# Kernel optimization log

Measured on AMD Instinct MI355X. Metric: run time of the kernel, lower is better.

## Reference

```python
import jax, jax.numpy as jnp
import numpy as np

N, E, D, C = 40000, 640000, 128, 64


def setup_inputs() -> dict:
    key = jax.random.key(0)
    ks = jax.random.split(key, 12)
    x = jax.random.normal(ks[0], (N, D), dtype=jnp.float32)
    edge_row = jax.random.randint(ks[1], (E,), 0, N, dtype=jnp.int32)
    edge_col = jax.random.randint(ks[2], (E,), 0, N, dtype=jnp.int32)
    edge_val = jax.random.uniform(ks[3], (E,), dtype=jnp.float32)
    s1 = 1.0 / np.sqrt(D)
    W1 = jax.random.uniform(ks[4], (D, D), minval=-s1, maxval=s1, dtype=jnp.float32)
    b1 = jax.random.uniform(ks[5], (D,), minval=-s1, maxval=s1, dtype=jnp.float32)
    W2 = jax.random.uniform(ks[6], (D, D), minval=-s1, maxval=s1, dtype=jnp.float32)
    b2 = jax.random.uniform(ks[7], (D,), minval=-s1, maxval=s1, dtype=jnp.float32)
    Wf = jax.random.uniform(ks[8], (D, C), minval=-s1, maxval=s1, dtype=jnp.float32)
    bf = jax.random.uniform(ks[9], (C,), minval=-s1, maxval=s1, dtype=jnp.float32)
    return {"x": x, "edge_row": edge_row, "edge_col": edge_col, "edge_val": edge_val,
            "W1": W1, "b1": b1, "W2": W2, "b2": b2, "Wf": Wf, "bf": bf}


def _spmm(row, col, val, dense):
    # out[row] += val * dense[col]  == adj @ dense with adj in COO form
    msgs = dense[col] * val[:, None]  # [E, D]
    return jax.ops.segment_sum(msgs, row, num_segments=N)


def reference(x, edge_row, edge_col, edge_val, W1, b1, W2, b2, Wf, bf):
    # gc1: relu(adj @ (x @ W1) + b1)
    h = jax.nn.relu(_spmm(edge_row, edge_col, edge_val, x @ W1) + b1)
    # dropout(p=0.2, training=False) -> identity in eval mode
    # gc2 + residual: relu(adj @ (h @ W2) + b2) + h
    h2 = jax.nn.relu(_spmm(edge_row, edge_col, edge_val, h @ W2) + b2) + h
    # final linear classifier
    return h2 @ Wf + bf
```

## Files before the change

### kernel.cpp

```cpp
#include <hip/hip_runtime.h>

#define N_NODES 40000
#define N_EDGES 640000
#define DIM     128
#define NCLS    64
#define CAP     64
#define CSTRIDE 16

typedef __attribute__((ext_vector_type(8))) short short8v;
typedef __attribute__((ext_vector_type(4))) float f32x4;

__device__ __forceinline__ unsigned short f2bf(float f) {
    unsigned int u = __float_as_uint(f);
    unsigned int r = u + 0x7fffu + ((u >> 16) & 1u);
    return (unsigned short)(r >> 16);
}
__device__ __forceinline__ float bf2f(unsigned int s) {
    return __uint_as_float(s << 16);
}

__launch_bounds__(256)
__global__ void prep(const float4* __restrict__ x4, uint2* __restrict__ xb,
                     const float* __restrict__ W1, const float* __restrict__ W2,
                     const float* __restrict__ Wf,
                     unsigned short* __restrict__ wt1, unsigned short* __restrict__ wt2,
                     unsigned short* __restrict__ wtf, int* __restrict__ counts) {
    const int b = blockIdx.x, tid = threadIdx.x;
    if (b < 5000) {
        int i = b * 256 + tid;
        float4 v = x4[i];
        uint2 o;
        o.x = (unsigned)f2bf(v.x) | ((unsigned)f2bf(v.y) << 16);
        o.y = (unsigned)f2bf(v.z) | ((unsigned)f2bf(v.w) << 16);
        xb[i] = o;
    } else if (b < 7500) {
        counts[(b - 5000) * 256 + tid] = 0;
    } else if (b < 7564) {
        int e = (b - 7500) * 256 + tid;
        int k = e >> 7, n = e & 127;
        wt1[n * 128 + k] = f2bf(W1[e]);
    } else if (b < 7628) {
        int e = (b - 7564) * 256 + tid;
        int k = e >> 7, n = e & 127;
        wt2[n * 128 + k] = f2bf(W2[e]);
    } else {
        int e = (b - 7628) * 256 + tid;
        int k = e >> 6, n = e & 63;
        wtf[n * 128 + k] = f2bf(Wf[e]);
    }
}

__launch_bounds__(256)
__global__ void build_bucket(const int* __restrict__ erow, const int* __restrict__ ecol,
                             const float* __restrict__ evalv, int* __restrict__ counts,
                             uint2* __restrict__ bslot) {
    int e = blockIdx.x * blockDim.x + threadIdx.x;
    if (e >= N_EDGES) return;
    int r = erow[e];
    int p = atomicAdd(&counts[r * CSTRIDE], 1);
    if (p < CAP)
        bslot[(size_t)r * CAP + p] = make_uint2((unsigned)ecol[e], __float_as_uint(evalv[e]));
}

__launch_bounds__(256)
__global__ void gemm_bf16_128(const unsigned short* __restrict__ A,
                              const unsigned short* __restrict__ WT,
                              unsigned short* __restrict__ C) {
    __shared__ unsigned short sB[128 * 128];
    const int tid = threadIdx.x;
    for (int c = tid; c < 2048; c += 256) {
        int n = c >> 4, j = c & 15;
        short8v v = *reinterpret_cast<const short8v*>(WT + n * 128 + 8 * j);
        *reinterpret_cast<short8v*>(&sB[n * 128 + 8 * (j ^ (n & 7))]) = v;
    }
    __syncthreads();

    const int lane = tid & 63;
    const int wv   = tid >> 6;
    const int m0   = blockIdx.x * 64 + wv * 16;
    const int r    = lane & 15;
    const int g    = lane >> 4;

    short8v af[4];
    const unsigned short* arow = A + (size_t)(m0 + r) * 128 + 8 * g;
#pragma unroll
    for (int f = 0; f < 4; ++f)
        af[f] = *reinterpret_cast<const short8v*>(arow + 32 * f);

    f32x4 acc[8];
#pragma unroll
    for (int nt = 0; nt < 8; ++nt) acc[nt] = (f32x4){0.f, 0.f, 0.f, 0.f};

#pragma unroll
    for (int nt = 0; nt < 8; ++nt) {
        const int rw = nt * 16 + r;
        const unsigned short* bbase = &sB[rw * 128];
#pragma unroll
        for (int f = 0; f < 4; ++f) {
            short8v bfr = *reinterpret_cast<const short8v*>(bbase + 8 * ((4 * f + g) ^ (rw & 7)));
            acc[nt] = __builtin_amdgcn_mfma_f32_16x16x32_bf16(af[f], bfr, acc[nt], 0, 0, 0);
        }
    }
#pragma unroll
    for (int nt = 0; nt < 8; ++nt)
#pragma unroll
        for (int rr = 0; rr < 4; ++rr)
            C[(size_t)(m0 + g * 4 + rr) * 128 + nt * 16 + r] = f2bf(acc[nt][rr]);
}

__launch_bounds__(256)
__global__ void gemm_bf16_final(const unsigned short* __restrict__ A,
                                const unsigned short* __restrict__ WT,
                                const float* __restrict__ bias,
                                float* __restrict__ C) {
    __shared__ unsigned short sB[64 * 128];
    const int tid = threadIdx.x;
    for (int c = tid; c < 1024; c += 256) {
        int n = c >> 4, j = c & 15;
        short8v v = *reinterpret_cast<const short8v*>(WT + n * 128 + 8 * j);
        *reinterpret_cast<short8v*>(&sB[n * 128 + 8 * (j ^ (n & 7))]) = v;
    }
    __syncthreads();

    const int lane = tid & 63;
    const int wv   = tid >> 6;
    const int m0   = blockIdx.x * 64 + wv * 16;
    const int r    = lane & 15;
    const int g    = lane >> 4;

    short8v af[4];
    const unsigned short* arow = A + (size_t)(m0 + r) * 128 + 8 * g;
#pragma unroll
    for (int f = 0; f < 4; ++f)
        af[f] = *reinterpret_cast<const short8v*>(arow + 32 * f);

    f32x4 acc[4];
#pragma unroll
    for (int nt = 0; nt < 4; ++nt) acc[nt] = (f32x4){0.f, 0.f, 0.f, 0.f};

#pragma unroll
    for (int nt = 0; nt < 4; ++nt) {
        const int rw = nt * 16 + r;
        const unsigned short* bbase = &sB[rw * 128];
#pragma unroll
        for (int f = 0; f < 4; ++f) {
            short8v bfr = *reinterpret_cast<const short8v*>(bbase + 8 * ((4 * f + g) ^ (rw & 7)));
            acc[nt] = __builtin_amdgcn_mfma_f32_16x16x32_bf16(af[f], bfr, acc[nt], 0, 0, 0);
        }
    }
#pragma unroll
    for (int nt = 0; nt < 4; ++nt)
#pragma unroll
        for (int rr = 0; rr < 4; ++rr)
            C[(size_t)(m0 + g * 4 + rr) * 64 + nt * 16 + r] = acc[nt][rr] + bias[nt * 16 + r];
}

__launch_bounds__(256)
__global__ void spmm_fused_bf16(const unsigned int* __restrict__ dense,
                                const uint2* __restrict__ bslot,
                                const int* __restrict__ counts,
                                const float* __restrict__ bias,
                                const float* __restrict__ resid,
                                float* __restrict__ out_f32,
                                unsigned int* __restrict__ out_bf) {
    const int lane = threadIdx.x & 63;
    const int wv   = threadIdx.x >> 6;
    const int row  = blockIdx.x * 4 + wv;
    int deg = counts[row * CSTRIDE];
    if (deg > CAP) deg = CAP;
    const size_t base = (size_t)row * CAP;

    int   colr = 0;
    float valr = 0.f;
    if (lane < deg) {
        uint2 s = bslot[base + lane];
        colr = (int)s.x;
        valr = __uint_as_float(s.y);
    }
    const int degUp = (deg + 3) & ~3;

    float ax0 = 0.f, ay0 = 0.f, ax1 = 0.f, ay1 = 0.f;
    float ax2 = 0.f, ay2 = 0.f, ax3 = 0.f, ay3 = 0.f;
    for (int i = 0; i < degUp; i += 4) {
        int   c0 = __shfl(colr, i + 0); float v0 = __shfl(valr, i + 0);
        int   c1 = __shfl(colr, i + 1); float v1 = __shfl(valr, i + 1);
        int   c2 = __shfl(colr, i + 2); float v2 = __shfl(valr, i + 2);
        int   c3 = __shfl(colr, i + 3); float v3 = __shfl(valr, i + 3);
        unsigned u0 = dense[(size_t)c0 * 64 + lane];
        unsigned u1 = dense[(size_t)c1 * 64 + lane];
        unsigned u2 = dense[(size_t)c2 * 64 + lane];
        unsigned u3 = dense[(size_t)c3 * 64 + lane];
        ax0 += v0 * bf2f(u0 & 0xffffu); ay0 += v0 * bf2f(u0 >> 16);
        ax1 += v1 * bf2f(u1 & 0xffffu); ay1 += v1 * bf2f(u1 >> 16);
        ax2 += v2 * bf2f(u2 & 0xffffu); ay2 += v2 * bf2f(u2 >> 16);
        ax3 += v3 * bf2f(u3 & 0xffffu); ay3 += v3 * bf2f(u3 >> 16);
    }
    float rx = (ax0 + ax1) + (ax2 + ax3);
    float ry = (ay0 + ay1) + (ay2 + ay3);

    const float2 bb = reinterpret_cast<const float2*>(bias)[lane];
    rx = fmaxf(rx + bb.x, 0.f);
    ry = fmaxf(ry + bb.y, 0.f);
    if (resid) {
        const float2 rr = reinterpret_cast<const float2*>(resid)[(size_t)row * 64 + lane];
        rx += rr.x; ry += rr.y;
    }
    if (out_f32)
        reinterpret_cast<float2*>(out_f32)[(size_t)row * 64 + lane] = make_float2(rx, ry);
    out_bf[(size_t)row * 64 + lane] = (unsigned)f2bf(rx) | ((unsigned)f2bf(ry) << 16);
}

extern "C" void kernel_launch(void* const* d_in, const int* in_sizes, int n_in,
                              void* d_out, int out_size, void* d_ws, size_t ws_size,
                              hipStream_t stream) {
    const float* x    = (const float*)d_in[0];
    const int*   erow = (const int*)  d_in[1];
    const int*   ecol = (const int*)  d_in[2];
    const float* ev   = (const float*)d_in[3];
    const float* W1   = (const float*)d_in[4];
    const float* b1   = (const float*)d_in[5];
    const float* W2   = (const float*)d_in[6];
    const float* b2   = (const float*)d_in[7];
    const float* Wf   = (const float*)d_in[8];
    const float* bf   = (const float*)d_in[9];
    float* out = (float*)d_out;

    const size_t MB = 1u << 20;
    char* ws = (char*)d_ws;
    int*            counts = (int*)           (ws + 0 * MB);
    uint2*          bslot  = (uint2*)         (ws + 4 * MB);
    unsigned short* xb     = (unsigned short*)(ws + 25 * MB);
    unsigned short* gb     = (unsigned short*)(ws + 36 * MB);
    unsigned short* hb     = (unsigned short*)(ws + 47 * MB);
    unsigned short* h2b    = (unsigned short*)(ws + 58 * MB);
    float*          hf     = (float*)         (ws + 69 * MB);
    unsigned short* wt1    = (unsigned short*)(ws + 90 * MB);
    unsigned short* wt2    = (unsigned short*)(ws + 90 * MB + 65536);
    unsigned short* wtf    = (unsigned short*)(ws + 90 * MB + 131072);

    prep<<<7660, 256, 0, stream>>>((const float4*)x, (uint2*)xb, W1, W2, Wf,
                                   wt1, wt2, wtf, counts);
    build_bucket<<<(N_EDGES + 255) / 256, 256, 0, stream>>>(erow, ecol, ev, counts, bslot);

    gemm_bf16_128<<<N_NODES / 64, 256, 0, stream>>>(xb, wt1, gb);
    spmm_fused_bf16<<<N_NODES / 4, 256, 0, stream>>>((const unsigned int*)gb, bslot, counts,
                                                     b1, nullptr, hf, (unsigned int*)hb);
    gemm_bf16_128<<<N_NODES / 64, 256, 0, stream>>>(hb, wt2, gb);
    spmm_fused_bf16<<<N_NODES / 4, 256, 0, stream>>>((const unsigned int*)gb, bslot, counts,
                                                     b2, hf, nullptr, (unsigned int*)h2b);
    gemm_bf16_final<<<N_NODES / 64, 256, 0, stream>>>(h2b, wtf, bf, out);
}
```

Baseline: 198.1 us.

## Fuse x conversion into first GEMM, use bf16 residual, split SpMM edges across half-waves

The first GEMM now reads fp32 x directly and converts it to bf16 in registers, which removes the separate x-to-bf16 pass from the prep kernel. The fp32 copy of h is no longer written; the residual in the second SpMM is read from the bf16 h buffer, cutting global traffic but adding another bf16 rounding to the residual. The SpMM has each half-wave handle alternate edges, with every lane loading 4 bf16 features (8 bytes), then combines the two halves with a cross-lane shuffle. This doubles the gathers in flight per wave, at the cost of padding degree up to a multiple of 8.

```diff
diff --git a/kernel.cpp b/kernel.cpp
--- a/kernel.cpp
+++ b/kernel.cpp
@@ -18,33 +18,29 @@
 __device__ __forceinline__ float bf2f(unsigned int s) {
     return __uint_as_float(s << 16);
 }
-
-__launch_bounds__(256)
-__global__ void prep(const float4* __restrict__ x4, uint2* __restrict__ xb,
-                     const float* __restrict__ W1, const float* __restrict__ W2,
+__device__ __forceinline__ float4 dec4(uint2 u) {
+    return make_float4(bf2f(u.x & 0xffffu), bf2f(u.x >> 16),
+                       bf2f(u.y & 0xffffu), bf2f(u.y >> 16));
+}
+
+__launch_bounds__(256)
+__global__ void prep(const float* __restrict__ W1, const float* __restrict__ W2,
                      const float* __restrict__ Wf,
                      unsigned short* __restrict__ wt1, unsigned short* __restrict__ wt2,
                      unsigned short* __restrict__ wtf, int* __restrict__ counts) {
     const int b = blockIdx.x, tid = threadIdx.x;
-    if (b < 5000) {
-        int i = b * 256 + tid;
-        float4 v = x4[i];
-        uint2 o;
-        o.x = (unsigned)f2bf(v.x) | ((unsigned)f2bf(v.y) << 16);
-        o.y = (unsigned)f2bf(v.z) | ((unsigned)f2bf(v.w) << 16);
-        xb[i] = o;
-    } else if (b < 7500) {
-        counts[(b - 5000) * 256 + tid] = 0;
-    } else if (b < 7564) {
-        int e = (b - 7500) * 256 + tid;
+    if (b < 2500) {
+        counts[b * 256 + tid] = 0;
+    } else if (b < 2564) {
+        int e = (b - 2500) * 256 + tid;
         int k = e >> 7, n = e & 127;
         wt1[n * 128 + k] = f2bf(W1[e]);
-    } else if (b < 7628) {
-        int e = (b - 7564) * 256 + tid;
+    } else if (b < 2628) {
+        int e = (b - 2564) * 256 + tid;
         int k = e >> 7, n = e & 127;
         wt2[n * 128 + k] = f2bf(W2[e]);
     } else {
-        int e = (b - 7628) * 256 + tid;
+        int e = (b - 2628) * 256 + tid;
         int k = e >> 6, n = e & 63;
         wtf[n * 128 + k] = f2bf(Wf[e]);
     }
@@ -60,6 +56,60 @@
     int p = atomicAdd(&counts[r * CSTRIDE], 1);
     if (p < CAP)
         bslot[(size_t)r * CAP + p] = make_uint2((unsigned)ecol[e], __float_as_uint(evalv[e]));
+}
+
+__launch_bounds__(256)
+__global__ void gemm_f32A_bf16(const float* __restrict__ A,
+                               const unsigned short* __restrict__ WT,
+                               unsigned short* __restrict__ C) {
+    __shared__ unsigned short sB[128 * 128];
+    const int tid = threadIdx.x;
+    for (int c = tid; c < 2048; c += 256) {
+        int n = c >> 4, j = c & 15;
+        short8v v = *reinterpret_cast<const short8v*>(WT + n * 128 + 8 * j);
+        *reinterpret_cast<short8v*>(&sB[n * 128 + 8 * (j ^ (n & 7))]) = v;
+    }
+    __syncthreads();
+
+    const int lane = tid & 63;
+    const int wv   = tid >> 6;
+    const int m0   = blockIdx.x * 64 + wv * 16;
+    const int r    = lane & 15;
+    const int g    = lane >> 4;
+
+    short8v af[4];
+    const float* arow = A + (size_t)(m0 + r) * 128 + 8 * g;
+#pragma unroll
+    for (int f = 0; f < 4; ++f) {
+        float4 p = *reinterpret_cast<const float4*>(arow + 32 * f);
+        float4 q = *reinterpret_cast<const float4*>(arow + 32 * f + 4);
+        short8v a;
+        a[0] = (short)f2bf(p.x); a[1] = (short)f2bf(p.y);
+        a[2] = (short)f2bf(p.z); a[3] = (short)f2bf(p.w);
+        a[4] = (short)f2bf(q.x); a[5] = (short)f2bf(q.y);
+        a[6] = (short)f2bf(q.z); a[7] = (short)f2bf(q.w);
+        af[f] = a;
+    }
+
+    f32x4 acc[8];
+#pragma unroll
+    for (int nt = 0; nt < 8; ++nt) acc[nt] = (f32x4){0.f, 0.f, 0.f, 0.f};
+
+#pragma unroll
+    for (int nt = 0; nt < 8; ++nt) {
+        const int rw = nt * 16 + r;
+        const unsigned short* bbase = &sB[rw * 128];
+#pragma unroll
+        for (int f = 0; f < 4; ++f) {
+            short8v bfr = *reinterpret_cast<const short8v*>(bbase + 8 * ((4 * f + g) ^ (rw & 7)));
+            acc[nt] = __builtin_amdgcn_mfma_f32_16x16x32_bf16(af[f], bfr, acc[nt], 0, 0, 0);
+        }
+    }
+#pragma unroll
+    for (int nt = 0; nt < 8; ++nt)
+#pragma unroll
+        for (int rr = 0; rr < 4; ++rr)
+            C[(size_t)(m0 + g * 4 + rr) * 128 + nt * 16 + r] = f2bf(acc[nt][rr]);
 }
 
 __launch_bounds__(256)
@@ -156,58 +206,69 @@
 }
 
 __launch_bounds__(256)
-__global__ void spmm_fused_bf16(const unsigned int* __restrict__ dense,
+__global__ void spmm_fused_bf16(const uint2* __restrict__ dense2,
                                 const uint2* __restrict__ bslot,
                                 const int* __restrict__ counts,
-                                const float* __restrict__ bias,
-                                const float* __restrict__ resid,
-                                float* __restrict__ out_f32,
-                                unsigned int* __restrict__ out_bf) {
+                                const float4* __restrict__ bias4,
+                                const uint2* __restrict__ residbf,
+                                uint2* __restrict__ outbf) {
     const int lane = threadIdx.x & 63;
-    const int wv   = threadIdx.x >> 6;
-    const int row  = blockIdx.x * 4 + wv;
+    const int half = lane >> 5;
+    const int sub  = lane & 31;
+    const int row  = blockIdx.x * 4 + (threadIdx.x >> 6);
     int deg = counts[row * CSTRIDE];
     if (deg > CAP) deg = CAP;
-    const size_t base = (size_t)row * CAP;
 
     int   colr = 0;
     float valr = 0.f;
     if (lane < deg) {
-        uint2 s = bslot[base + lane];
+        uint2 s = bslot[(size_t)row * CAP + lane];
         colr = (int)s.x;
         valr = __uint_as_float(s.y);
     }
-    const int degUp = (deg + 3) & ~3;
-
-    float ax0 = 0.f, ay0 = 0.f, ax1 = 0.f, ay1 = 0.f;
-    float ax2 = 0.f, ay2 = 0.f, ax3 = 0.f, ay3 = 0.f;
-    for (int i = 0; i < degUp; i += 4) {
-        int   c0 = __shfl(colr, i + 0); float v0 = __shfl(valr, i + 0);
-        int   c1 = __shfl(colr, i + 1); float v1 = __shfl(valr, i + 1);
-        int   c2 = __shfl(colr, i + 2); float v2 = __shfl(valr, i + 2);
-        int   c3 = __shfl(colr, i + 3); float v3 = __shfl(valr, i + 3);
-        unsigned u0 = dense[(size_t)c0 * 64 + lane];
-        unsigned u1 = dense[(size_t)c1 * 64 + lane];
-        unsigned u2 = dense[(size_t)c2 * 64 + lane];
-        unsigned u3 = dense[(size_t)c3 * 64 + lane];
-        ax0 += v0 * bf2f(u0 & 0xffffu); ay0 += v0 * bf2f(u0 >> 16);
-        ax1 += v1 * bf2f(u1 & 0xffffu); ay1 += v1 * bf2f(u1 >> 16);
-        ax2 += v2 * bf2f(u2 & 0xffffu); ay2 += v2 * bf2f(u2 >> 16);
-        ax3 += v3 * bf2f(u3 & 0xffffu); ay3 += v3 * bf2f(u3 >> 16);
-    }
-    float rx = (ax0 + ax1) + (ax2 + ax3);
-    float ry = (ay0 + ay1) + (ay2 + ay3);
-
-    const float2 bb = reinterpret_cast<const float2*>(bias)[lane];
-    rx = fmaxf(rx + bb.x, 0.f);
-    ry = fmaxf(ry + bb.y, 0.f);
-    if (resid) {
-        const float2 rr = reinterpret_cast<const float2*>(resid)[(size_t)row * 64 + lane];
-        rx += rr.x; ry += rr.y;
-    }
-    if (out_f32)
-        reinterpret_cast<float2*>(out_f32)[(size_t)row * 64 + lane] = make_float2(rx, ry);
-    out_bf[(size_t)row * 64 + lane] = (unsigned)f2bf(rx) | ((unsigned)f2bf(ry) << 16);
+    const int degUp = (deg + 7) & ~7;
+
+    float ax0 = 0.f, ay0 = 0.f, az0 = 0.f, aw0 = 0.f;
+    float ax1 = 0.f, ay1 = 0.f, az1 = 0.f, aw1 = 0.f;
+    float ax2 = 0.f, ay2 = 0.f, az2 = 0.f, aw2 = 0.f;
+    float ax3 = 0.f, ay3 = 0.f, az3 = 0.f, aw3 = 0.f;
+    for (int i = 0; i < degUp; i += 8) {
+        int   c0 = __shfl(colr, i + 0 + half); float v0 = __shfl(valr, i + 0 + half);
+        int   c1 = __shfl(colr, i + 2 + half); float v1 = __shfl(valr, i + 2 + half);
+        int   c2 = __shfl(colr, i + 4 + half); float v2 = __shfl(valr, i + 4 + half);
+        int   c3 = __shfl(colr, i + 6 + half); float v3 = __shfl(valr, i + 6 + half);
+        uint2 u0 = dense2[(size_t)c0 * 32 + sub];
+        uint2 u1 = dense2[(size_t)c1 * 32 + sub];
+        uint2 u2 = dense2[(size_t)c2 * 32 + sub];
+        uint2 u3 = dense2[(size_t)c3 * 32 + sub];
+        float4 d0 = dec4(u0); ax0 += v0 * d0.x; ay0 += v0 * d0.y; az0 += v0 * d0.z; aw0 += v0 * d0.w;
+        float4 d1 = dec4(u1); ax1 += v1 * d1.x; ay1 += v1 * d1.y; az1 += v1 * d1.z; aw1 += v1 * d1.w;
+        float4 d2 = dec4(u2); ax2 += v2 * d2.x; ay2 += v2 * d2.y; az2 += v2 * d2.z; aw2 += v2 * d2.w;
+        float4 d3 = dec4(u3); ax3 += v3 * d3.x; ay3 += v3 * d3.y; az3 += v3 * d3.z; aw3 += v3 * d3.w;
+    }
+    float sx = (ax0 + ax1) + (ax2 + ax3);
+    float sy = (ay0 + ay1) + (ay2 + ay3);
+    float sz = (az0 + az1) + (az2 + az3);
+    float sw = (aw0 + aw1) + (aw2 + aw3);
+    sx += __shfl_xor(sx, 32);
+    sy += __shfl_xor(sy, 32);
+    sz += __shfl_xor(sz, 32);
+    sw += __shfl_xor(sw, 32);
+
+    if (half == 0) {
+        float4 bb = bias4[sub];
+        sx = fmaxf(sx + bb.x, 0.f);
+        sy = fmaxf(sy + bb.y, 0.f);
+        sz = fmaxf(sz + bb.z, 0.f);
+        sw = fmaxf(sw + bb.w, 0.f);
+        if (residbf) {
+            float4 rr = dec4(residbf[(size_t)row * 32 + sub]);
+            sx += rr.x; sy += rr.y; sz += rr.z; sw += rr.w;
+        }
+        outbf[(size_t)row * 32 + sub] =
+            make_uint2((unsigned)f2bf(sx) | ((unsigned)f2bf(sy) << 16),
+                       (unsigned)f2bf(sz) | ((unsigned)f2bf(sw) << 16));
+    }
 }
 
 extern "C" void kernel_launch(void* const* d_in, const int* in_sizes, int n_in,
@@ -229,24 +290,23 @@
     char* ws = (char*)d_ws;
     int*            counts = (int*)           (ws + 0 * MB);
     uint2*          bslot  = (uint2*)         (ws + 4 * MB);
-    unsigned short* xb     = (unsigned short*)(ws + 25 * MB);
-    unsigned short* gb     = (unsigned short*)(ws + 36 * MB);
-    unsigned short* hb     = (unsigned short*)(ws + 47 * MB);
-    unsigned short* h2b    = (unsigned short*)(ws + 58 * MB);
-    float*          hf     = (float*)         (ws + 69 * MB);
-    unsigned short* wt1    = (unsigned short*)(ws + 90 * MB);
-    unsigned short* wt2    = (unsigned short*)(ws + 90 * MB + 65536);
-    unsigned short* wtf    = (unsigned short*)(ws + 90 * MB + 131072);
-
-    prep<<<7660, 256, 0, stream>>>((const float4*)x, (uint2*)xb, W1, W2, Wf,
-                                   wt1, wt2, wtf, counts);
+    unsigned short* gb     = (unsigned short*)(ws + 25 * MB);
+    unsigned short* hb     = (unsigned short*)(ws + 36 * MB);
+    unsigned short* h2b    = (unsigned short*)(ws + 47 * MB);
+    unsigned short* wt1    = (unsigned short*)(ws + 58 * MB);
+    unsigned short* wt2    = (unsigned short*)(ws + 58 * MB + 65536);
+    unsigned short* wtf    = (unsigned short*)(ws + 58 * MB + 131072);
+
+    prep<<<2660, 256, 0, stream>>>(W1, W2, Wf, wt1, wt2, wtf, counts);
     build_bucket<<<(N_EDGES + 255) / 256, 256, 0, stream>>>(erow, ecol, ev, counts, bslot);
 
-    gemm_bf16_128<<<N_NODES / 64, 256, 0, stream>>>(xb, wt1, gb);
-    spmm_fused_bf16<<<N_NODES / 4, 256, 0, stream>>>((const unsigned int*)gb, bslot, counts,
-                                                     b1, nullptr, hf, (unsigned int*)hb);
+    gemm_f32A_bf16<<<N_NODES / 64, 256, 0, stream>>>(x, wt1, gb);
+    spmm_fused_bf16<<<N_NODES / 4, 256, 0, stream>>>((const uint2*)gb, bslot, counts,
+                                                     (const float4*)b1, nullptr,
+                                                     (uint2*)hb);
     gemm_bf16_128<<<N_NODES / 64, 256, 0, stream>>>(hb, wt2, gb);
-    spmm_fused_bf16<<<N_NODES / 4, 256, 0, stream>>>((const unsigned int*)gb, bslot, counts,
-                                                     b2, hf, nullptr, (unsigned int*)h2b);
+    spmm_fused_bf16<<<N_NODES / 4, 256, 0, stream>>>((const uint2*)gb, bslot, counts,
+                                                     (const float4*)b2, (const uint2*)hb,
+                                                     (uint2*)h2b);
     gemm_bf16_final<<<N_NODES / 64, 256, 0, stream>>>(h2b, wtf, bf, out);
 }
```

Result: faster. 188.0 us (-5.1%).
